# Kernel tuning notes

Hardware: AMD Instinct MI355X
Metric: run time of the kernel (lower is better)

Reference implementation:

```python
import jax, jax.numpy as jnp
import numpy as np
from jax import lax

L = 1024       # sequence length
D = 64         # bond_dim
O = 128        # output_dim
P = 2          # d_phys
B = 4096       # batch
SPLIT = L // 2


def _ident(dl, dr):
    # identity boost added to every physical slice: t[k, p, k] += 1 for k < min(dl, dr)
    m = min(dl, dr)
    base = jnp.zeros((dl, dr), dtype=jnp.float32)
    base = base.at[jnp.arange(m), jnp.arange(m)].set(1.0)
    return base[:, None, :]  # (dl, 1, dr) broadcast over p


def setup_inputs() -> dict:
    key = jax.random.key(0)
    k0, k1, k2, k3, k4, k5 = jax.random.split(key, 6)
    x = jax.random.uniform(k0, (B, L), dtype=jnp.float32)
    left0 = jax.random.normal(k1, (1, P, D), dtype=jnp.float32) * 0.01 + _ident(1, D)
    left_rest = jax.random.normal(k2, (SPLIT - 1, D, P, D), dtype=jnp.float32) * 0.01 + _ident(D, D)[None]
    center = jax.random.normal(k3, (D, D, O), dtype=jnp.float32) / jnp.sqrt(jnp.float32(O))
    right_rest = jax.random.normal(k4, (L - SPLIT - 1, D, P, D), dtype=jnp.float32) * 0.01 + _ident(D, D)[None]
    right_last = jax.random.normal(k5, (D, P, 1), dtype=jnp.float32) * 0.01 + _ident(D, 1)
    return {"x": x, "left0": left0, "left_rest": left_rest, "center": center,
            "right_rest": right_rest, "right_last": right_last}


def _norm_env(env):
    return env / (jnp.linalg.norm(env, axis=1, keepdims=True) + 1e-8)


def reference(x, left0, left_rest, center, right_rest, right_last):
    angle = (jnp.pi / 2.0) * x
    phi = jnp.stack([jnp.cos(angle), jnp.sin(angle)], axis=-1)  # (B, L, P)

    # left sweep: first tensor has trivial left bond (=1)
    left = _norm_env(jnp.einsum('pr,bp->br', left0[0], phi[:, 0]))

    def lstep(env, inp):
        A, p = inp  # A: (D,P,D), p: (B,P)
        return _norm_env(jnp.einsum('bl,lpr,bp->br', env, A, p)), None

    phi_l = jnp.swapaxes(phi[:, 1:SPLIT], 0, 1)  # (SPLIT-1, B, P)
    left, _ = lax.scan(lstep, left, (left_rest, phi_l))

    # right sweep (from last site inward): last tensor has trivial right bond (=1)
    right = _norm_env(jnp.einsum('lp,bp->bl', right_last[:, :, 0], phi[:, L - 1]))

    def rstep(env, inp):
        A, p = inp
        return _norm_env(jnp.einsum('br,lpr,bp->bl', env, A, p)), None

    phi_r = jnp.swapaxes(phi[:, SPLIT:L - 1], 0, 1)[::-1]  # reversed order
    right, _ = lax.scan(rstep, right, (right_rest[::-1], phi_r))

    out = jnp.einsum('bl,br,lro->bo', left, right, center)  # (B, O)
    # F.normalize(p=2, dim=1) with eps=1e-12
    return out / jnp.clip(jnp.linalg.norm(out, axis=1, keepdims=True), 1e-12)
```

## Files before the change

### kernel.cpp

```cpp
#include <hip/hip_runtime.h>

typedef float vf4 __attribute__((ext_vector_type(4)));
typedef int vi4 __attribute__((ext_vector_type(4)));
typedef int vi2 __attribute__((ext_vector_type(2)));
typedef short short8 __attribute__((ext_vector_type(8)));
typedef unsigned short ushort8 __attribute__((ext_vector_type(8)));

#define LL 1024
#define DD 64
#define OO 128
#define BBATCH 4096
#define NS 511
#define SITE_F 8192

__device__ __forceinline__ void gld_lds16(const float* g, float* l) {
  __builtin_amdgcn_global_load_lds(
      (const __attribute__((address_space(1))) unsigned int*)g,
      (__attribute__((address_space(3))) unsigned int*)l, 16, 0, 0);
}

__device__ __forceinline__ unsigned short f2bf(float v) {
  const unsigned uu = __builtin_bit_cast(unsigned, v);
  return (unsigned short)((uu + 0x7FFFu + ((uu >> 16) & 1u)) >> 16);
}

__global__ __launch_bounds__(256) void prep(const float* __restrict__ lsrc,
                                            const float* __restrict__ rsrc,
                                            unsigned short* __restrict__ Wl,
                                            unsigned short* __restrict__ Wr) {
  __shared__ float S[SITE_F];
  const int site = blockIdx.x;
  const int dir = blockIdx.y;
  const int tid = threadIdx.x;
  const float* src = (dir ? rsrc : lsrc) + (size_t)site * SITE_F;
  unsigned short* dst = dir ? (Wr + (size_t)(NS - 1 - site) * SITE_F)
                            : (Wl + (size_t)site * SITE_F);
#pragma unroll
  for (int m = 0; m < 8; m++)
    *(vf4*)&S[(m * 256 + tid) * 4] = *(const vf4*)&src[(m * 256 + tid) * 4];
  __syncthreads();
#pragma unroll
  for (int q = 0; q < 4; q++) {
    const int slot = q * 256 + tid;
    const int lane = slot & 63, f = slot >> 6;
    const int mt = f >> 2, s = f & 3;
    const int g = lane >> 4, c = lane & 15;
    const int m = 16 * mt + c;
    ushort8 t;
#pragma unroll
    for (int j = 0; j < 8; j++) {
      const int k = 32 * s + 8 * g + j;
      float v;
      if (dir == 0) {
        const int l = k >> 1, p = k & 1;
        v = S[l * 128 + p * 64 + m] - ((m == l) ? 1.f : 0.f);
      } else {
        const int r = k >> 1, p = k & 1;
        v = S[m * 128 + p * 64 + r] - ((m == r) ? 1.f : 0.f);
      }
      t[j] = f2bf(v);
    }
    *(ushort8*)&dst[(size_t)slot * 8] = t;
  }
}

__global__ __launch_bounds__(256) void prep2(const float* __restrict__ center,
                                             unsigned short* __restrict__ Cf) {
  __shared__ float S[4096];
  const int o = blockIdx.x;
  const int tid = threadIdx.x;
#pragma unroll
  for (int k = 0; k < 16; k++) {
    const int idx = k * 256 + tid;
    S[idx] = center[(size_t)idx * 128 + o];
  }
  __syncthreads();
#pragma unroll
  for (int q = 0; q < 2; q++) {
    const int slot = q * 256 + tid;
    const int lane = slot & 63, f = slot >> 6;
    const int mt = f >> 1, s = f & 1;
    const int g = lane >> 4, c = lane & 15;
    const int l = 16 * mt + c;
    ushort8 t;
#pragma unroll
    for (int j = 0; j < 8; j++) {
      const int r = 32 * s + 8 * g + j;
      t[j] = f2bf(S[l * 64 + r]);
    }
    *(ushort8*)&Cf[(size_t)((o * 8 + f) * 64 + lane) * 8] = t;
  }
}

#define STAGE_GROUP(G, BUF)                                                    \
  {                                                                            \
    _Pragma("unroll")                                                          \
    for (int s4 = 0; s4 < 4; s4++) {                                           \
      int st_ = (G) * 4 + s4;                                                  \
      if (st_ > NS - 1) st_ = NS - 1;                                          \
      const float* Ws_ = Wf + (size_t)st_ * 4096;                              \
      float* d_ = &ring[BUF][s4][0];                                           \
      _Pragma("unroll")                                                        \
      for (int q = 0; q < 8; q++)                                              \
        gld_lds16(Ws_ + q * 512 + tid * 4, d_ + q * 512 + tid * 4);            \
    }                                                                          \
  }

#define LOAD_FC(FC, RB)                                                        \
  {                                                                            \
    const float* rb_ = (RB);                                                   \
    _Pragma("unroll")                                                          \
    for (int q = 0; q < 16; q++)                                               \
      FC[q] = *(const vf4*)&rb_[(q * 64 + lane) * 4];                          \
  }

#define BODYP(I, FCc, FCn, RBN, PF)                                            \
  {                                                                            \
    if (PF) {                                                                  \
      LOAD_FC(FCn, RBN)                                                        \
      __builtin_amdgcn_sched_barrier(0);                                       \
    }                                                                          \
    const int nI = (I) + 1;                                                    \
    float xn = 0.f;                                                            \
    if (nI <= NS - 1) xn = xrow[dir ? (1022 - nI) : (1 + nI)];                 \
    short8 e2[4];                                                              \
    _Pragma("unroll")                                                          \
    for (int s = 0; s < 4; s++) {                                              \
      int pk[4];                                                               \
      _Pragma("unroll")                                                        \
      for (int t = 0; t < 4; t++) {                                            \
        const float f0 = u[s][t] * CS, f1 = u[s][t] * SN;                      \
        int p;                                                                 \
        asm("v_cvt_pk_bf16_f32 %0, %1, %2" : "=v"(p) : "v"(f0), "v"(f1));      \
        pk[t] = p;                                                             \
      }                                                                        \
      e2[s] = __builtin_bit_cast(short8, (vi4){pk[0], pk[1], pk[2], pk[3]});   \
    }                                                                          \
    const float keff = CS + SN;                                                \
    vf4 accA[4], accB[4];                                                      \
    _Pragma("unroll")                                                          \
    for (int mt = 0; mt < 4; mt++) {                                           \
      vf4 z;                                                                   \
      z[0] = keff * u[mt][0]; z[1] = keff * u[mt][1];                          \
      z[2] = keff * u[mt][2]; z[3] = keff * u[mt][3];                          \
      accA[mt] = z;                                                            \
      accB[mt] = (vf4){0.f, 0.f, 0.f, 0.f};                                    \
    }                                                                          \
    _Pragma("unroll")                                                          \
    for (int mt = 0; mt < 4; mt++) {                                           \
      accA[mt] = __builtin_amdgcn_mfma_f32_16x16x32_bf16(                      \
          __builtin_bit_cast(short8, FCc[mt * 4 + 0]), e2[0], accA[mt], 0,0,0);\
      accA[mt] = __builtin_amdgcn_mfma_f32_16x16x32_bf16(                      \
          __builtin_bit_cast(short8, FCc[mt * 4 + 1]), e2[1], accA[mt], 0,0,0);\
      accB[mt] = __builtin_amdgcn_mfma_f32_16x16x32_bf16(                      \
          __builtin_bit_cast(short8, FCc[mt * 4 + 2]), e2[2], accB[mt], 0,0,0);\
      accB[mt] = __builtin_amdgcn_mfma_f32_16x16x32_bf16(                      \
          __builtin_bit_cast(short8, FCc[mt * 4 + 3]), e2[3], accB[mt], 0,0,0);\
    }                                                                          \
    _Pragma("unroll")                                                          \
    for (int mt = 0; mt < 4; mt++) u[mt] = accA[mt] + accB[mt];                \
    if (nI <= NS - 1) {                                                        \
      const float qrev = 0.25f * xn;           \
      float c_, s_;                                                            \
      asm("v_cos_f32 %0, %1" : "=v"(c_) : "v"(qrev));                          \
      asm("v_sin_f32 %0, %1" : "=v"(s_) : "v"(qrev));                          \
      CS = c_;                                                                 \
      SN = s_;                                                                 \
    }                                                                          \
    if (((I) & 7) == 7) {                              \
      float nss = 0.f;                                                         \
      _Pragma("unroll")                                                        \
      for (int mt = 0; mt < 4; mt++)                                           \
        _Pragma("unroll")                                                      \
        for (int r = 0; r < 4; r++) nss += u[mt][r] * u[mt][r];                \
      nss += __shfl_xor(nss, 16);                                              \
      nss += __shfl_xor(nss, 32);                                              \
      const int eb = (__float_as_int(nss) >> 23) & 0xFF;                       \
      const float alpha = __int_as_float((127 - ((eb - 127) >> 1)) << 23);     \
      _Pragma("unroll")                                                        \
      for (int mt = 0; mt < 4; mt++)                                           \
        _Pragma("unroll")                                                      \
        for (int r = 0; r < 4; r++) u[mt][r] *= alpha;                         \
    }                                                                          \
  }

__global__ __launch_bounds__(128, 1) void sweep(const float* __restrict__ x,
                                                const float* __restrict__ left0,
                                                const float* __restrict__ right_last,
                                                const unsigned short* __restrict__ Wl,
                                                const unsigned short* __restrict__ Wr,
                                                float* __restrict__ envL,
                                                float* __restrict__ envR,
                                                unsigned short* __restrict__ Lb16,
                                                unsigned short* __restrict__ Rb16) {
  __shared__ float ring[2][4][4096];
  const int bid = blockIdx.x;
  const int xcd = bid & 7;
  const int dir = xcd >> 2;
  const int slot = (xcd & 3) * 32 + (bid >> 3);
  const int tid = threadIdx.x;
  const int wave = tid >> 6;
  const int lane = tid & 63;
  const int g_ = lane >> 4, c = lane & 15;
  const int b = (slot * 2 + wave) * 16 + c;
  const float* xrow = x + (size_t)b * LL;

  const float* Wf = (const float*)(dir ? Wr : Wl);

  vf4 u[4];
  {
    const float x0 = xrow[dir ? (LL - 1) : 0];
    const float qrev = 0.25f * x0;
    float cs, sn;
    asm("v_cos_f32 %0, %1" : "=v"(cs) : "v"(qrev));
    asm("v_sin_f32 %0, %1" : "=v"(sn) : "v"(qrev));
#pragma unroll
    for (int mt = 0; mt < 4; mt++)
#pragma unroll
      for (int r = 0; r < 4; r++) {
        const int n = 16 * mt + 4 * g_ + r;
        const float w0 = dir ? right_last[n * 2] : left0[n];
        const float w1 = dir ? right_last[n * 2 + 1] : left0[64 + n];
        u[mt][r] = cs * w0 + sn * w1;
      }
    float ss = 0.f;
#pragma unroll
    for (int mt = 0; mt < 4; mt++)
#pragma unroll
      for (int r = 0; r < 4; r++) ss += u[mt][r] * u[mt][r];
    ss += __shfl_xor(ss, 16);
    ss += __shfl_xor(ss, 32);
    const float a0 = 1.f / (sqrtf(ss) + 1e-8f);
#pragma unroll
    for (int mt = 0; mt < 4; mt++)
#pragma unroll
      for (int r = 0; r < 4; r++) u[mt][r] *= a0;
  }

  float CS, SN;
  {
    const float q0 = 0.25f * xrow[dir ? 1022 : 1];
    asm("v_cos_f32 %0, %1" : "=v"(CS) : "v"(q0));
    asm("v_sin_f32 %0, %1" : "=v"(SN) : "v"(q0));
  }

  STAGE_GROUP(0, 0)
  __syncthreads();

  vf4 fX[16], fY[16];
  for (int g = 0; g < 127; g++) {
    const int buf = g & 1;
    LOAD_FC(fX, &ring[buf][0][0])
    STAGE_GROUP(g + 1, buf ^ 1)
    const int i0 = g * 4;
    BODYP(i0 + 0, fX, fY, &ring[buf][1][0], 1)
    BODYP(i0 + 1, fY, fX, &ring[buf][2][0], 1)
    BODYP(i0 + 2, fX, fY, &ring[buf][3][0], 1)
    BODYP(i0 + 3, fY, fX, &ring[buf][0][0], 0)
    __syncthreads();
  }
  LOAD_FC(fX, &ring[1][0][0])
  BODYP(508, fX, fY, &ring[1][1][0], 1)
  BODYP(509, fY, fX, &ring[1][2][0], 1)
  BODYP(510, fX, fY, &ring[1][3][0], 0)

  float nss = 0.f;
#pragma unroll
  for (int mt = 0; mt < 4; mt++)
#pragma unroll
    for (int r = 0; r < 4; r++) nss += u[mt][r] * u[mt][r];
  nss += __shfl_xor(nss, 16);
  nss += __shfl_xor(nss, 32);
  const float alpha = 1.f / (sqrtf(nss) + 1e-8f);

  float* eo = (dir ? envR : envL) + (size_t)b * 64;
  unsigned short* eo16 = (dir ? Rb16 : Lb16) + (size_t)b * 64;
#pragma unroll
  for (int mt = 0; mt < 4; mt++) {
    vf4 v;
#pragma unroll
    for (int r = 0; r < 4; r++) v[r] = u[mt][r] * alpha;
    *(vf4*)&eo[16 * mt + 4 * g_] = v;
    int p01, p23;
    asm("v_cvt_pk_bf16_f32 %0, %1, %2" : "=v"(p01) : "v"(v[0]), "v"(v[1]));
    asm("v_cvt_pk_bf16_f32 %0, %1, %2" : "=v"(p23) : "v"(v[2]), "v"(v[3]));
    *(vi2*)&eo16[16 * mt + 4 * g_] = (vi2){p01, p23};
  }
}

__global__ __launch_bounds__(256) void centerk2(const float* __restrict__ envL,
                                                const unsigned short* __restrict__ Rb16,
                                                const unsigned short* __restrict__ Cf,
                                                float* __restrict__ Pp) {
  const int b0 = blockIdx.x * 16;
  const int tid = threadIdx.x;
  const int wave = tid >> 6;
  const int lane = tid & 63;
  const int g = lane >> 4, c = lane & 15;

  short8 rf[2];
#pragma unroll
  for (int s = 0; s < 2; s++)
    rf[s] = __builtin_bit_cast(short8,
        *(const ushort8*)&Rb16[(size_t)(b0 + c) * 64 + 32 * s + 8 * g]);

  vf4 Lv[4];
#pragma unroll
  for (int mt = 0; mt < 4; mt++)
    Lv[mt] = *(const vf4*)&envL[(size_t)(b0 + c) * 64 + 16 * mt + 4 * g];

  for (int oi = 0; oi < 32; oi++) {
    const int o = wave * 32 + oi;
    const unsigned short* cb = Cf + (size_t)(o * 8) * 64 * 8;
    vf4 acc[4];
#pragma unroll
    for (int mt = 0; mt < 4; mt++) {
      const short8 a0 = __builtin_bit_cast(short8,
          *(const ushort8*)&cb[(size_t)((mt * 2 + 0) * 64 + lane) * 8]);
      const short8 a1 = __builtin_bit_cast(short8,
          *(const ushort8*)&cb[(size_t)((mt * 2 + 1) * 64 + lane) * 8]);
      vf4 z = {0.f, 0.f, 0.f, 0.f};
      z = __builtin_amdgcn_mfma_f32_16x16x32_bf16(a0, rf[0], z, 0, 0, 0);
      z = __builtin_amdgcn_mfma_f32_16x16x32_bf16(a1, rf[1], z, 0, 0, 0);
      acc[mt] = z;
    }
    float ps = 0.f;
#pragma unroll
    for (int mt = 0; mt < 4; mt++)
#pragma unroll
      for (int r = 0; r < 4; r++) ps += Lv[mt][r] * acc[mt][r];
    ps += __shfl_xor(ps, 16);
    ps += __shfl_xor(ps, 32);
    if (g == 0) Pp[(size_t)(b0 + c) * 128 + o] = ps;
  }
}

__global__ __launch_bounds__(256) void combinek2(const float* __restrict__ P,
                                                 float* __restrict__ out) {
  const int row = blockIdx.x * 8 + (threadIdx.x >> 5);
  const int o0 = (threadIdx.x & 31) * 4;
  vf4 v = *(const vf4*)&P[(size_t)row * 128 + o0];
  float ss = v[0] * v[0] + v[1] * v[1] + v[2] * v[2] + v[3] * v[3];
#pragma unroll
  for (int m = 1; m < 32; m <<= 1) ss += __shfl_xor(ss, m);
  const float inv = 1.f / fmaxf(sqrtf(ss), 1e-12f);
  v *= inv;
  *(vf4*)&out[(size_t)row * 128 + o0] = v;
}

extern "C" void kernel_launch(void* const* d_in, const int* in_sizes, int n_in,
                              void* d_out, int out_size, void* d_ws, size_t ws_size,
                              hipStream_t stream) {
  const float* x = (const float*)d_in[0];
  const float* left0 = (const float*)d_in[1];
  const float* left_rest = (const float*)d_in[2];
  const float* center = (const float*)d_in[3];
  const float* right_rest = (const float*)d_in[4];
  const float* right_last = (const float*)d_in[5];
  float* out = (float*)d_out;

  char* wsb = (char*)d_ws;
  unsigned short* Wl = (unsigned short*)wsb;
  unsigned short* Wr = Wl + (size_t)NS * SITE_F;
  float* envL = (float*)(Wr + (size_t)NS * SITE_F);
  float* envR = envL + (size_t)BBATCH * 64;
  unsigned short* Lb16 = (unsigned short*)(envR + (size_t)BBATCH * 64);
  unsigned short* Rb16 = Lb16 + (size_t)BBATCH * 64;
  unsigned short* Cf = Rb16 + (size_t)BBATCH * 64;
  float* Pp = (float*)(Cf + (size_t)OO * 8 * 64 * 8);

  hipLaunchKernelGGL(prep, dim3(NS, 2), dim3(256), 0, stream,
                     left_rest, right_rest, Wl, Wr);
  hipLaunchKernelGGL(prep2, dim3(OO), dim3(256), 0, stream, center, Cf);
  hipLaunchKernelGGL(sweep, dim3(256), dim3(128), 0, stream,
                     x, left0, right_last, Wl, Wr, envL, envR, Lb16, Rb16);
  hipLaunchKernelGGL(centerk2, dim3(BBATCH / 16), dim3(256), 0, stream,
                     envL, Rb16, Cf, Pp);
  hipLaunchKernelGGL(combinek2, dim3(BBATCH / 8), dim3(256), 0, stream, Pp, out);
}
```

Before: 320.2 us.

## Fuse adjacent MPS sites into pair tensors to halve sequential sweep steps

A new prep kernel contracts each pair of neighbouring site tensors into a combined (D, P*P, D) tensor stored in bf16 MFMA fragment layout. The sweep then applies one K=256 MFMA chain per pair instead of two K=128 steps, so the serial dependency chain is half as long and each step carries more work. This trades extra prep FLOPs, a doubled per-step fragment load (32 vf4 registers), and extra bf16 rounding of the fused product. The unused bf16 left-environment output is also dropped.

```diff
diff --git a/kernel.cpp b/kernel.cpp
--- a/kernel.cpp
+++ b/kernel.cpp
@@ -7,11 +7,13 @@
 typedef unsigned short ushort8 __attribute__((ext_vector_type(8)));
 
 #define LL 1024
-#define DD 64
 #define OO 128
 #define BBATCH 4096
 #define NS 511
+#define NP 256
 #define SITE_F 8192
+#define PAIR_U16 16384
+#define PAIR_F 8192
 
 __device__ __forceinline__ void gld_lds16(const float* g, float* l) {
   __builtin_amdgcn_global_load_lds(
@@ -24,43 +26,94 @@
   return (unsigned short)((uu + 0x7FFFu + ((uu >> 16) & 1u)) >> 16);
 }
 
-__global__ __launch_bounds__(256) void prep(const float* __restrict__ lsrc,
-                                            const float* __restrict__ rsrc,
-                                            unsigned short* __restrict__ Wl,
-                                            unsigned short* __restrict__ Wr) {
-  __shared__ float S[SITE_F];
-  const int site = blockIdx.x;
-  const int dir = blockIdx.y;
+__global__ __launch_bounds__(256) void prep_pair(const float* __restrict__ lsrc,
+                                                 const float* __restrict__ rsrc,
+                                                 unsigned short* __restrict__ Wp) {
+  __shared__ float X[8192];
+  __shared__ float YT[8192];
+  const int pair = blockIdx.x, dir = blockIdx.y;
   const int tid = threadIdx.x;
-  const float* src = (dir ? rsrc : lsrc) + (size_t)site * SITE_F;
-  unsigned short* dst = dir ? (Wr + (size_t)(NS - 1 - site) * SITE_F)
-                            : (Wl + (size_t)site * SITE_F);
-#pragma unroll
-  for (int m = 0; m < 8; m++)
-    *(vf4*)&S[(m * 256 + tid) * 4] = *(const vf4*)&src[(m * 256 + tid) * 4];
+  unsigned short* dst = Wp + ((size_t)dir * NP + pair) * PAIR_U16;
+  const bool ph = (pair == NP - 1);
+
+  const float* Xg;
+  const float* Yg = nullptr;
+  if (dir == 0) {
+    Xg = lsrc + (size_t)(2 * pair) * SITE_F;
+    if (!ph) Yg = lsrc + (size_t)(2 * pair + 1) * SITE_F;
+  } else {
+    const int s1 = 510 - 2 * pair;
+    if (!ph) {
+      Xg = rsrc + (size_t)(s1 - 1) * SITE_F;
+      Yg = rsrc + (size_t)s1 * SITE_F;
+    } else {
+      Xg = rsrc;
+    }
+  }
+#pragma unroll
+  for (int q8 = 0; q8 < 8; q8++)
+    *(vf4*)&X[(q8 * 256 + tid) * 4] = *(const vf4*)&Xg[(q8 * 256 + tid) * 4];
+  if (!ph) {
+#pragma unroll
+    for (int q8 = 0; q8 < 8; q8++) {
+      const int e = (q8 * 256 + tid) * 4;
+      const vf4 v = *(const vf4*)&Yg[e];
+      const int A = e >> 7, B = (e >> 6) & 1, C = e & 63;
+#pragma unroll
+      for (int k2 = 0; k2 < 4; k2++)
+        YT[(B * 64 + C + k2) * 64 + A] = v[k2];
+    }
+  }
   __syncthreads();
-#pragma unroll
-  for (int q = 0; q < 4; q++) {
-    const int slot = q * 256 + tid;
-    const int lane = slot & 63, f = slot >> 6;
-    const int mt = f >> 2, s = f & 3;
-    const int g = lane >> 4, c = lane & 15;
-    const int m = 16 * mt + c;
-    ushort8 t;
-#pragma unroll
-    for (int j = 0; j < 8; j++) {
-      const int k = 32 * s + 8 * g + j;
-      float v;
-      if (dir == 0) {
-        const int l = k >> 1, p = k & 1;
-        v = S[l * 128 + p * 64 + m] - ((m == l) ? 1.f : 0.f);
+
+  const int kk = tid >> 2;
+  const int p = (tid >> 1) & 1, q = tid & 1;
+  const int s = 2 * (kk >> 4) + p;
+  const int g = (kk >> 2) & 3;
+  const int j = 2 * (kk & 3) + q;
+
+  vf4 row[16];
+  if (dir == 0) {
+#pragma unroll
+    for (int w = 0; w < 16; w++)
+      row[w] = *(const vf4*)&X[kk * 128 + p * 64 + w * 4];
+  } else if (!ph) {
+#pragma unroll
+    for (int w = 0; w < 16; w++)
+      row[w] = *(const vf4*)&YT[(p * 64 + kk) * 64 + w * 4];
+  }
+
+  for (int mm = 0; mm < 64; mm++) {
+    float val;
+    if (dir == 0) {
+      if (!ph) {
+        float d = 0.f;
+#pragma unroll
+        for (int w = 0; w < 16; w++) {
+          const vf4 y = *(const vf4*)&YT[(q * 64 + mm) * 64 + w * 4];
+          d += row[w][0] * y[0] + row[w][1] * y[1] +
+               row[w][2] * y[2] + row[w][3] * y[3];
+        }
+        val = d - ((kk == mm) ? 1.f : 0.f);
       } else {
-        const int r = k >> 1, p = k & 1;
-        v = S[m * 128 + p * 64 + r] - ((m == r) ? 1.f : 0.f);
+        val = row[mm >> 2][mm & 3] - ((kk == mm) ? 1.f : 0.f);
       }
-      t[j] = f2bf(v);
-    }
-    *(ushort8*)&dst[(size_t)slot * 8] = t;
+    } else {
+      if (!ph) {
+        float d = 0.f;
+#pragma unroll
+        for (int w = 0; w < 16; w++) {
+          const vf4 xv = *(const vf4*)&X[mm * 128 + q * 64 + w * 4];
+          d += xv[0] * row[w][0] + xv[1] * row[w][1] +
+               xv[2] * row[w][2] + xv[3] * row[w][3];
+        }
+        val = d - ((mm == kk) ? 1.f : 0.f);
+      } else {
+        val = X[mm * 128 + p * 64 + kk] - ((mm == kk) ? 1.f : 0.f);
+      }
+    }
+    const int mt = mm >> 4, c = mm & 15;
+    dst[(size_t)(((mt * 8 + s) * 64) + (g << 4) + c) * 8 + j] = f2bf(val);
   }
 }
 
@@ -95,79 +148,73 @@
 #define STAGE_GROUP(G, BUF)                                                    \
   {                                                                            \
     _Pragma("unroll")                                                          \
-    for (int s4 = 0; s4 < 4; s4++) {                                           \
-      int st_ = (G) * 4 + s4;                                                  \
-      if (st_ > NS - 1) st_ = NS - 1;                                          \
-      const float* Ws_ = Wf + (size_t)st_ * 4096;                              \
-      float* d_ = &ring[BUF][s4][0];                                           \
+    for (int s2 = 0; s2 < 2; s2++) {                                           \
+      const float* src_ = Wf + (size_t)(2 * (G) + s2) * PAIR_F;                \
+      float* d_ = &ring[BUF][s2][0];                                           \
       _Pragma("unroll")                                                        \
-      for (int q = 0; q < 8; q++)                                              \
-        gld_lds16(Ws_ + q * 512 + tid * 4, d_ + q * 512 + tid * 4);            \
-    }                                                                          \
-  }
-
-#define LOAD_FC(FC, RB)                                                        \
+      for (int q8 = 0; q8 < 16; q8++)                                          \
+        gld_lds16(src_ + q8 * 512 + tid * 4, d_ + q8 * 512 + tid * 4);         \
+    }                                                                          \
+  }
+
+#define PBODY(PR, BUF, S2)                                                     \
   {                                                                            \
-    const float* rb_ = (RB);                                                   \
+    const int pr_ = (PR);                                                      \
+    const float* rb = &ring[BUF][S2][0];                                       \
+    vf4 FC[32];                                                                \
     _Pragma("unroll")                                                          \
-    for (int q = 0; q < 16; q++)                                               \
-      FC[q] = *(const vf4*)&rb_[(q * 64 + lane) * 4];                          \
-  }
-
-#define BODYP(I, FCc, FCn, RBN, PF)                                            \
-  {                                                                            \
-    if (PF) {                                                                  \
-      LOAD_FC(FCn, RBN)                                                        \
-      __builtin_amdgcn_sched_barrier(0);                                       \
-    }                                                                          \
-    const int nI = (I) + 1;                                                    \
-    float xn = 0.f;                                                            \
-    if (nI <= NS - 1) xn = xrow[dir ? (1022 - nI) : (1 + nI)];                 \
-    short8 e2[4];                                                              \
-    _Pragma("unroll")                                                          \
-    for (int s = 0; s < 4; s++) {                                              \
-      int pk[4];                                                               \
-      _Pragma("unroll")                                                        \
-      for (int t = 0; t < 4; t++) {                                            \
-        const float f0 = u[s][t] * CS, f1 = u[s][t] * SN;                      \
-        int p;                                                                 \
-        asm("v_cvt_pk_bf16_f32 %0, %1, %2" : "=v"(p) : "v"(f0), "v"(f1));      \
-        pk[t] = p;                                                             \
-      }                                                                        \
-      e2[s] = __builtin_bit_cast(short8, (vi4){pk[0], pk[1], pk[2], pk[3]});   \
-    }                                                                          \
-    const float keff = CS + SN;                                                \
-    vf4 accA[4], accB[4];                                                      \
+    for (int f = 0; f < 32; f++)                                               \
+      FC[f] = *(const vf4*)&rb[f * 256 + lane * 4];                            \
+    const int npr = pr_ + 1;                                                   \
+    float xiN = 0.f, xjN = 0.f;                                                \
+    if (npr < NP) {                                                            \
+      xiN = xrow[dir ? (1022 - 2 * npr) : (1 + 2 * npr)];                      \
+      xjN = (npr == NP - 1) ? 0.f                                              \
+                            : xrow[dir ? (1021 - 2 * npr) : (2 + 2 * npr)];    \
+    }                                                                          \
+    const float keff = (ci + si) * (cj + sj);                                  \
+    const float w00 = ci * cj, w01 = ci * sj;                                  \
+    const float w10 = si * cj, w11 = si * sj;                                  \
+    vf4 acc[4];                                                                \
     _Pragma("unroll")                                                          \
     for (int mt = 0; mt < 4; mt++) {                                           \
       vf4 z;                                                                   \
       z[0] = keff * u[mt][0]; z[1] = keff * u[mt][1];                          \
       z[2] = keff * u[mt][2]; z[3] = keff * u[mt][3];                          \
-      accA[mt] = z;                                                            \
-      accB[mt] = (vf4){0.f, 0.f, 0.f, 0.f};                                    \
+      acc[mt] = z;                                                             \
     }                                                                          \
     _Pragma("unroll")                                                          \
-    for (int mt = 0; mt < 4; mt++) {                                           \
-      accA[mt] = __builtin_amdgcn_mfma_f32_16x16x32_bf16(                      \
-          __builtin_bit_cast(short8, FCc[mt * 4 + 0]), e2[0], accA[mt], 0,0,0);\
-      accA[mt] = __builtin_amdgcn_mfma_f32_16x16x32_bf16(                      \
-          __builtin_bit_cast(short8, FCc[mt * 4 + 1]), e2[1], accA[mt], 0,0,0);\
-      accB[mt] = __builtin_amdgcn_mfma_f32_16x16x32_bf16(                      \
-          __builtin_bit_cast(short8, FCc[mt * 4 + 2]), e2[2], accB[mt], 0,0,0);\
-      accB[mt] = __builtin_amdgcn_mfma_f32_16x16x32_bf16(                      \
-          __builtin_bit_cast(short8, FCc[mt * 4 + 3]), e2[3], accB[mt], 0,0,0);\
+    for (int s = 0; s < 8; s++) {                                              \
+      const float wa = (s & 1) ? w10 : w00;                                    \
+      const float wb = (s & 1) ? w11 : w01;                                    \
+      int pk[4];                                                               \
+      _Pragma("unroll")                                                        \
+      for (int t = 0; t < 4; t++) {                                            \
+        const float f0 = u[s >> 1][t] * wa, f1 = u[s >> 1][t] * wb;            \
+        int pp;                                                                \
+        asm("v_cvt_pk_bf16_f32 %0, %1, %2" : "=v"(pp) : "v"(f0), "v"(f1));     \
+        pk[t] = pp;                                                            \
+      }                                                                        \
+      const short8 e2s =                                                       \
+          __builtin_bit_cast(short8, (vi4){pk[0], pk[1], pk[2], pk[3]});       \
+      _Pragma("unroll")                                                        \
+      for (int mt = 0; mt < 4; mt++)                                           \
+        acc[mt] = __builtin_amdgcn_mfma_f32_16x16x32_bf16(                     \
+            __builtin_bit_cast(short8, FC[mt * 8 + s]), e2s, acc[mt], 0, 0, 0);\
     }                                                                          \
     _Pragma("unroll")                                                          \
-    for (int mt = 0; mt < 4; mt++) u[mt] = accA[mt] + accB[mt];                \
-    if (nI <= NS - 1) {                                                        \
-      const float qrev = 0.25f * xn;           \
+    for (int mt = 0; mt < 4; mt++) u[mt] = acc[mt];                            \
+    if (npr < NP) {                                                            \
+      const float qi = 0.25f * xiN, qj = 0.25f * xjN;                          \
       float c_, s_;                                                            \
-      asm("v_cos_f32 %0, %1" : "=v"(c_) : "v"(qrev));                          \
-      asm("v_sin_f32 %0, %1" : "=v"(s_) : "v"(qrev));                          \
-      CS = c_;                                                                 \
-      SN = s_;                                                                 \
-    }                                                                          \
-    if (((I) & 7) == 7) {                              \
+      asm("v_cos_f32 %0, %1" : "=v"(c_) : "v"(qi));                            \
+      asm("v_sin_f32 %0, %1" : "=v"(s_) : "v"(qi));                            \
+      ci = c_; si = s_;                                                        \
+      asm("v_cos_f32 %0, %1" : "=v"(c_) : "v"(qj));                            \
+      asm("v_sin_f32 %0, %1" : "=v"(s_) : "v"(qj));                            \
+      cj = c_; sj = s_;                                                        \
+    }                                                                          \
+    if ((pr_ & 3) == 3) {              \
       float nss = 0.f;                                                         \
       _Pragma("unroll")                                                        \
       for (int mt = 0; mt < 4; mt++)                                           \
@@ -187,13 +234,11 @@
 __global__ __launch_bounds__(128, 1) void sweep(const float* __restrict__ x,
                                                 const float* __restrict__ left0,
                                                 const float* __restrict__ right_last,
-                                                const unsigned short* __restrict__ Wl,
-                                                const unsigned short* __restrict__ Wr,
+                                                const unsigned short* __restrict__ Wp,
                                                 float* __restrict__ envL,
                                                 float* __restrict__ envR,
-                                                unsigned short* __restrict__ Lb16,
                                                 unsigned short* __restrict__ Rb16) {
-  __shared__ float ring[2][4][4096];
+  __shared__ float ring[2][2][PAIR_F];
   const int bid = blockIdx.x;
   const int xcd = bid & 7;
   const int dir = xcd >> 2;
@@ -205,7 +250,7 @@
   const int b = (slot * 2 + wave) * 16 + c;
   const float* xrow = x + (size_t)b * LL;
 
-  const float* Wf = (const float*)(dir ? Wr : Wl);
+  const float* Wf = (const float*)(Wp + (size_t)dir * NP * PAIR_U16);
 
   vf4 u[4];
   {
@@ -237,32 +282,27 @@
       for (int r = 0; r < 4; r++) u[mt][r] *= a0;
   }
 
-  float CS, SN;
+  STAGE_GROUP(0, 0)
+
+  float ci, si, cj, sj;
   {
-    const float q0 = 0.25f * xrow[dir ? 1022 : 1];
-    asm("v_cos_f32 %0, %1" : "=v"(CS) : "v"(q0));
-    asm("v_sin_f32 %0, %1" : "=v"(SN) : "v"(q0));
-  }
-
-  STAGE_GROUP(0, 0)
+    const float xi = xrow[dir ? 1022 : 1];
+    const float xj = xrow[dir ? 1021 : 2];
+    const float qi = 0.25f * xi, qj = 0.25f * xj;
+    asm("v_cos_f32 %0, %1" : "=v"(ci) : "v"(qi));
+    asm("v_sin_f32 %0, %1" : "=v"(si) : "v"(qi));
+    asm("v_cos_f32 %0, %1" : "=v"(cj) : "v"(qj));
+    asm("v_sin_f32 %0, %1" : "=v"(sj) : "v"(qj));
+  }
   __syncthreads();
 
-  vf4 fX[16], fY[16];
-  for (int g = 0; g < 127; g++) {
+  for (int g = 0; g < 128; g++) {
     const int buf = g & 1;
-    LOAD_FC(fX, &ring[buf][0][0])
-    STAGE_GROUP(g + 1, buf ^ 1)
-    const int i0 = g * 4;
-    BODYP(i0 + 0, fX, fY, &ring[buf][1][0], 1)
-    BODYP(i0 + 1, fY, fX, &ring[buf][2][0], 1)
-    BODYP(i0 + 2, fX, fY, &ring[buf][3][0], 1)
-    BODYP(i0 + 3, fY, fX, &ring[buf][0][0], 0)
+    if (g < 127) STAGE_GROUP(g + 1, buf ^ 1)
+    PBODY(2 * g, buf, 0)
+    PBODY(2 * g + 1, buf, 1)
     __syncthreads();
   }
-  LOAD_FC(fX, &ring[1][0][0])
-  BODYP(508, fX, fY, &ring[1][1][0], 1)
-  BODYP(509, fY, fX, &ring[1][2][0], 1)
-  BODYP(510, fX, fY, &ring[1][3][0], 0)
 
   float nss = 0.f;
 #pragma unroll
@@ -274,17 +314,18 @@
   const float alpha = 1.f / (sqrtf(nss) + 1e-8f);
 
   float* eo = (dir ? envR : envL) + (size_t)b * 64;
-  unsigned short* eo16 = (dir ? Rb16 : Lb16) + (size_t)b * 64;
 #pragma unroll
   for (int mt = 0; mt < 4; mt++) {
     vf4 v;
 #pragma unroll
     for (int r = 0; r < 4; r++) v[r] = u[mt][r] * alpha;
     *(vf4*)&eo[16 * mt + 4 * g_] = v;
-    int p01, p23;
-    asm("v_cvt_pk_bf16_f32 %0, %1, %2" : "=v"(p01) : "v"(v[0]), "v"(v[1]));
-    asm("v_cvt_pk_bf16_f32 %0, %1, %2" : "=v"(p23) : "v"(v[2]), "v"(v[3]));
-    *(vi2*)&eo16[16 * mt + 4 * g_] = (vi2){p01, p23};
+    if (dir) {
+      int p01, p23;
+      asm("v_cvt_pk_bf16_f32 %0, %1, %2" : "=v"(p01) : "v"(v[0]), "v"(v[1]));
+      asm("v_cvt_pk_bf16_f32 %0, %1, %2" : "=v"(p23) : "v"(v[2]), "v"(v[3]));
+      *(vi2*)&Rb16[(size_t)b * 64 + 16 * mt + 4 * g_] = (vi2){p01, p23};
+    }
   }
 }
 
@@ -360,20 +401,18 @@
   float* out = (float*)d_out;
 
   char* wsb = (char*)d_ws;
-  unsigned short* Wl = (unsigned short*)wsb;
-  unsigned short* Wr = Wl + (size_t)NS * SITE_F;
-  float* envL = (float*)(Wr + (size_t)NS * SITE_F);
+  unsigned short* Wp = (unsigned short*)wsb;
+  float* envL = (float*)(Wp + (size_t)2 * NP * PAIR_U16);
   float* envR = envL + (size_t)BBATCH * 64;
-  unsigned short* Lb16 = (unsigned short*)(envR + (size_t)BBATCH * 64);
-  unsigned short* Rb16 = Lb16 + (size_t)BBATCH * 64;
+  unsigned short* Rb16 = (unsigned short*)(envR + (size_t)BBATCH * 64);
   unsigned short* Cf = Rb16 + (size_t)BBATCH * 64;
   float* Pp = (float*)(Cf + (size_t)OO * 8 * 64 * 8);
 
-  hipLaunchKernelGGL(prep, dim3(NS, 2), dim3(256), 0, stream,
-                     left_rest, right_rest, Wl, Wr);
+  hipLaunchKernelGGL(prep_pair, dim3(NP, 2), dim3(256), 0, stream,
+                     left_rest, right_rest, Wp);
   hipLaunchKernelGGL(prep2, dim3(OO), dim3(256), 0, stream, center, Cf);
   hipLaunchKernelGGL(sweep, dim3(256), dim3(128), 0, stream,
-                     x, left0, right_last, Wl, Wr, envL, envR, Lb16, Rb16);
+                     x, left0, right_last, Wp, envL, envR, Rb16);
   hipLaunchKernelGGL(centerk2, dim3(BBATCH / 16), dim3(256), 0, stream,
                      envL, Rb16, Cf, Pp);
   hipLaunchKernelGGL(combinek2, dim3(BBATCH / 8), dim3(256), 0, stream, Pp, out);
```

Measured after the change: 357.9 us. 11.8% more time.

## Use single-wave sweep blocks over 512 blocks with smaller LDS ring

Applied to the files above, without the earlier changes.

The sweep kernel now runs 512 blocks of one wave each instead of 256 blocks of two waves, so each block handles one 16-row batch tile in one direction. The LDS ring shrinks from two buffers of four sites to two buffers of two sites. The software-prefetch of the next site's weight fragments into a second register set is dropped in favour of loading them inside each step. This spreads the sequential sweep across more compute units and cuts LDS and register use per block, but it loses the register double-buffering, doubles weight staging traffic per batch row, and adds more barriers per site. The unused left-environment bf16 output is also removed.

```diff
diff --git a/kernel.cpp b/kernel.cpp
--- a/kernel.cpp
+++ b/kernel.cpp
@@ -7,7 +7,6 @@
 typedef unsigned short ushort8 __attribute__((ext_vector_type(8)));
 
 #define LL 1024
-#define DD 64
 #define OO 128
 #define BBATCH 4096
 #define NS 511
@@ -95,31 +94,24 @@
 #define STAGE_GROUP(G, BUF)                                                    \
   {                                                                            \
     _Pragma("unroll")                                                          \
-    for (int s4 = 0; s4 < 4; s4++) {                                           \
-      int st_ = (G) * 4 + s4;                                                  \
+    for (int s2 = 0; s2 < 2; s2++) {                                           \
+      int st_ = (G) * 2 + s2;                                                  \
       if (st_ > NS - 1) st_ = NS - 1;                                          \
-      const float* Ws_ = Wf + (size_t)st_ * 4096;                              \
-      float* d_ = &ring[BUF][s4][0];                                           \
+      const float* src_ = Wf + (size_t)st_ * 4096;                             \
+      float* d_ = &ring[BUF][s2][0];                                           \
       _Pragma("unroll")                                                        \
-      for (int q = 0; q < 8; q++)                                              \
-        gld_lds16(Ws_ + q * 512 + tid * 4, d_ + q * 512 + tid * 4);            \
-    }                                                                          \
-  }
-
-#define LOAD_FC(FC, RB)                                                        \
+      for (int q = 0; q < 16; q++)                                             \
+        gld_lds16(src_ + q * 256 + lane * 4, d_ + q * 256 + lane * 4);         \
+    }                                                                          \
+  }
+
+#define BODY(I, BUF, S2)                                                       \
   {                                                                            \
-    const float* rb_ = (RB);                                                   \
+    const float* rb = &ring[BUF][S2][0];                                       \
+    vf4 FC[16];                                                                \
     _Pragma("unroll")                                                          \
     for (int q = 0; q < 16; q++)                                               \
-      FC[q] = *(const vf4*)&rb_[(q * 64 + lane) * 4];                          \
-  }
-
-#define BODYP(I, FCc, FCn, RBN, PF)                                            \
-  {                                                                            \
-    if (PF) {                                                                  \
-      LOAD_FC(FCn, RBN)                                                        \
-      __builtin_amdgcn_sched_barrier(0);                                       \
-    }                                                                          \
+      FC[q] = *(const vf4*)&rb[(q * 64 + lane) * 4];                           \
     const int nI = (I) + 1;                                                    \
     float xn = 0.f;                                                            \
     if (nI <= NS - 1) xn = xrow[dir ? (1022 - nI) : (1 + nI)];                 \
@@ -149,13 +141,13 @@
     _Pragma("unroll")                                                          \
     for (int mt = 0; mt < 4; mt++) {                                           \
       accA[mt] = __builtin_amdgcn_mfma_f32_16x16x32_bf16(                      \
-          __builtin_bit_cast(short8, FCc[mt * 4 + 0]), e2[0], accA[mt], 0,0,0);\
+          __builtin_bit_cast(short8, FC[mt * 4 + 0]), e2[0], accA[mt], 0,0,0); \
       accA[mt] = __builtin_amdgcn_mfma_f32_16x16x32_bf16(                      \
-          __builtin_bit_cast(short8, FCc[mt * 4 + 1]), e2[1], accA[mt], 0,0,0);\
+          __builtin_bit_cast(short8, FC[mt * 4 + 1]), e2[1], accA[mt], 0,0,0); \
       accB[mt] = __builtin_amdgcn_mfma_f32_16x16x32_bf16(                      \
-          __builtin_bit_cast(short8, FCc[mt * 4 + 2]), e2[2], accB[mt], 0,0,0);\
+          __builtin_bit_cast(short8, FC[mt * 4 + 2]), e2[2], accB[mt], 0,0,0); \
       accB[mt] = __builtin_amdgcn_mfma_f32_16x16x32_bf16(                      \
-          __builtin_bit_cast(short8, FCc[mt * 4 + 3]), e2[3], accB[mt], 0,0,0);\
+          __builtin_bit_cast(short8, FC[mt * 4 + 3]), e2[3], accB[mt], 0,0,0); \
     }                                                                          \
     _Pragma("unroll")                                                          \
     for (int mt = 0; mt < 4; mt++) u[mt] = accA[mt] + accB[mt];                \
@@ -167,7 +159,7 @@
       CS = c_;                                                                 \
       SN = s_;                                                                 \
     }                                                                          \
-    if (((I) & 7) == 7) {                              \
+    if (((I) & 7) == 7) {         \
       float nss = 0.f;                                                         \
       _Pragma("unroll")                                                        \
       for (int mt = 0; mt < 4; mt++)                                           \
@@ -184,25 +176,22 @@
     }                                                                          \
   }
 
-__global__ __launch_bounds__(128, 1) void sweep(const float* __restrict__ x,
-                                                const float* __restrict__ left0,
-                                                const float* __restrict__ right_last,
-                                                const unsigned short* __restrict__ Wl,
-                                                const unsigned short* __restrict__ Wr,
-                                                float* __restrict__ envL,
-                                                float* __restrict__ envR,
-                                                unsigned short* __restrict__ Lb16,
-                                                unsigned short* __restrict__ Rb16) {
-  __shared__ float ring[2][4][4096];
+__global__ __launch_bounds__(64, 1) void sweep(const float* __restrict__ x,
+                                               const float* __restrict__ left0,
+                                               const float* __restrict__ right_last,
+                                               const unsigned short* __restrict__ Wl,
+                                               const unsigned short* __restrict__ Wr,
+                                               float* __restrict__ envL,
+                                               float* __restrict__ envR,
+                                               unsigned short* __restrict__ Rb16) {
+  __shared__ float ring[2][2][4096];
   const int bid = blockIdx.x;
   const int xcd = bid & 7;
   const int dir = xcd >> 2;
-  const int slot = (xcd & 3) * 32 + (bid >> 3);
-  const int tid = threadIdx.x;
-  const int wave = tid >> 6;
-  const int lane = tid & 63;
+  const int pr = (xcd & 3) * 64 + (bid >> 3);
+  const int lane = threadIdx.x;
   const int g_ = lane >> 4, c = lane & 15;
-  const int b = (slot * 2 + wave) * 16 + c;
+  const int b = pr * 16 + c;
   const float* xrow = x + (size_t)b * LL;
 
   const float* Wf = (const float*)(dir ? Wr : Wl);
@@ -247,22 +236,15 @@
   STAGE_GROUP(0, 0)
   __syncthreads();
 
-  vf4 fX[16], fY[16];
-  for (int g = 0; g < 127; g++) {
+  for (int g = 0; g < 255; g++) {
     const int buf = g & 1;
-    LOAD_FC(fX, &ring[buf][0][0])
     STAGE_GROUP(g + 1, buf ^ 1)
-    const int i0 = g * 4;
-    BODYP(i0 + 0, fX, fY, &ring[buf][1][0], 1)
-    BODYP(i0 + 1, fY, fX, &ring[buf][2][0], 1)
-    BODYP(i0 + 2, fX, fY, &ring[buf][3][0], 1)
-    BODYP(i0 + 3, fY, fX, &ring[buf][0][0], 0)
+    const int i0 = g * 2;
+    BODY(i0 + 0, buf, 0)
+    BODY(i0 + 1, buf, 1)
     __syncthreads();
   }
-  LOAD_FC(fX, &ring[1][0][0])
-  BODYP(508, fX, fY, &ring[1][1][0], 1)
-  BODYP(509, fY, fX, &ring[1][2][0], 1)
-  BODYP(510, fX, fY, &ring[1][3][0], 0)
+  BODY(510, 1, 0)
 
   float nss = 0.f;
 #pragma unroll
@@ -274,17 +256,18 @@
   const float alpha = 1.f / (sqrtf(nss) + 1e-8f);
 
   float* eo = (dir ? envR : envL) + (size_t)b * 64;
-  unsigned short* eo16 = (dir ? Rb16 : Lb16) + (size_t)b * 64;
 #pragma unroll
   for (int mt = 0; mt < 4; mt++) {
     vf4 v;
 #pragma unroll
     for (int r = 0; r < 4; r++) v[r] = u[mt][r] * alpha;
     *(vf4*)&eo[16 * mt + 4 * g_] = v;
-    int p01, p23;
-    asm("v_cvt_pk_bf16_f32 %0, %1, %2" : "=v"(p01) : "v"(v[0]), "v"(v[1]));
-    asm("v_cvt_pk_bf16_f32 %0, %1, %2" : "=v"(p23) : "v"(v[2]), "v"(v[3]));
-    *(vi2*)&eo16[16 * mt + 4 * g_] = (vi2){p01, p23};
+    if (dir) {
+      int p01, p23;
+      asm("v_cvt_pk_bf16_f32 %0, %1, %2" : "=v"(p01) : "v"(v[0]), "v"(v[1]));
+      asm("v_cvt_pk_bf16_f32 %0, %1, %2" : "=v"(p23) : "v"(v[2]), "v"(v[3]));
+      *(vi2*)&Rb16[(size_t)b * 64 + 16 * mt + 4 * g_] = (vi2){p01, p23};
+    }
   }
 }
 
@@ -364,16 +347,15 @@
   unsigned short* Wr = Wl + (size_t)NS * SITE_F;
   float* envL = (float*)(Wr + (size_t)NS * SITE_F);
   float* envR = envL + (size_t)BBATCH * 64;
-  unsigned short* Lb16 = (unsigned short*)(envR + (size_t)BBATCH * 64);
-  unsigned short* Rb16 = Lb16 + (size_t)BBATCH * 64;
+  unsigned short* Rb16 = (unsigned short*)(envR + (size_t)BBATCH * 64);
   unsigned short* Cf = Rb16 + (size_t)BBATCH * 64;
   float* Pp = (float*)(Cf + (size_t)OO * 8 * 64 * 8);
 
   hipLaunchKernelGGL(prep, dim3(NS, 2), dim3(256), 0, stream,
                      left_rest, right_rest, Wl, Wr);
   hipLaunchKernelGGL(prep2, dim3(OO), dim3(256), 0, stream, center, Cf);
-  hipLaunchKernelGGL(sweep, dim3(256), dim3(128), 0, stream,
-                     x, left0, right_last, Wl, Wr, envL, envR, Lb16, Rb16);
+  hipLaunchKernelGGL(sweep, dim3(512), dim3(64), 0, stream,
+                     x, left0, right_last, Wl, Wr, envL, envR, Rb16);
   hipLaunchKernelGGL(centerk2, dim3(BBATCH / 16), dim3(256), 0, stream,
                      envL, Rb16, Cf, Pp);
   hipLaunchKernelGGL(combinek2, dim3(BBATCH / 8), dim3(256), 0, stream, Pp, out);
```

Result: slower. 414.8 us (+29.5%).
